# Optimization experiments

Hardware: AMD Instinct MI355X
Metric: run time of the kernel (lower is better)

## Reference

```python
import jax, jax.numpy as jnp
import numpy as np

HID = 2048      # hidden_size
NH = 32         # num_heads
G = 8           # num_kv_groups
R = NH // G     # repeat factor (heads per kv group)
HD = HID // NH  # head_dim = 64
SCALE = HD ** 0.5


def setup_inputs() -> dict:
    key = jax.random.key(0)
    ks = jax.random.split(key, 10)
    B, S = 2, 1024
    x = jax.random.normal(ks[0], (B, S, HID), dtype=jnp.float32)
    attention_mask = jnp.ones((B, S, S), dtype=jnp.float32)
    # Linear params stored as [in, out] (y = x @ W + b), same math as torch Linear.
    Wq = jax.random.normal(ks[1], (HID, HID), dtype=jnp.float32) * 0.02
    bq = jnp.zeros((HID,), dtype=jnp.float32)
    Wk = jax.random.normal(ks[2], (HID, G * HD), dtype=jnp.float32) * 0.02
    bk = jnp.zeros((G * HD,), dtype=jnp.float32)
    Wv = jax.random.normal(ks[3], (HID, G * HD), dtype=jnp.float32) * 0.02
    bv = jnp.zeros((G * HD,), dtype=jnp.float32)
    Wo = jax.random.normal(ks[4], (HID, HID), dtype=jnp.float32) * 0.02
    bo = jnp.zeros((HID,), dtype=jnp.float32)
    return {"x": x, "attention_mask": attention_mask,
            "Wq": Wq, "bq": bq, "Wk": Wk, "bk": bk,
            "Wv": Wv, "bv": bv, "Wo": Wo, "bo": bo}


def reference(x, attention_mask, Wq, bq, Wk, bk, Wv, bv, Wo, bo):
    B, S, _ = x.shape
    # Projections. Group heads as (G, R) instead of repeat_interleave:
    # repeat_interleave(key, R, dim=2) duplicates each kv group R times, which is
    # exactly sharing key[:, :, g] across the R heads of group g.
    q = (x @ Wq + bq).reshape(B, S, G, R, HD)   # [B,S,G,R,HD] (heads = G*R in order)
    k = (x @ Wk + bk).reshape(B, S, G, HD)      # [B,S,G,HD]
    v = (x @ Wv + bv).reshape(B, S, G, HD)
    # scores [B,G,R,Sq,Sk] == torch's [B, NH, Sq, Sk] with NH = G*R
    scores = jnp.einsum('bqgrd,bkgd->bgrqk', q, k) / SCALE
    scores = scores * attention_mask[:, None, None]  # multiplicative mask per head
    w = jax.nn.softmax(scores, axis=-1)
    out = jnp.einsum('bgrqk,bkgd->bqgrd', w, v).reshape(B, S, HID)
    return out @ Wo + bo + x
```

## Files before the change

### kernel.cpp

```cpp
#include <hip/hip_runtime.h>

typedef unsigned short u16;
typedef unsigned int u32;
typedef __attribute__((ext_vector_type(8))) short bf16x8;
typedef __attribute__((ext_vector_type(4))) float f32x4;

#define HID 2048
#define S_LEN 1024
#define BATCH 2
#define G_KV 8
#define R_REP 4
#define HD 64
#define NQKV 3072

__device__ __forceinline__ u16 f2bf(float f) {
    union { u32 u; float ff; } x; x.ff = f;
    u32 u = x.u;
    u += 0x7FFFu + ((u >> 16) & 1u);
    return (u16)(u >> 16);
}

__device__ __forceinline__ void gload_lds16(const void* g, void* l) {
    __builtin_amdgcn_global_load_lds((const __attribute__((address_space(1))) void*)g,
                                     (__attribute__((address_space(3))) void*)l,
                                     16, 0, 0);
}

__global__ __launch_bounds__(256) void cvt_x(const float* __restrict__ in,
                                             u16* __restrict__ out) {
    int i = (blockIdx.x * 256 + threadIdx.x) * 8;
    float4 a = *(const float4*)(in + i);
    float4 b = *(const float4*)(in + i + 4);
    u16 t[8] = {f2bf(a.x), f2bf(a.y), f2bf(a.z), f2bf(a.w),
                f2bf(b.x), f2bf(b.y), f2bf(b.z), f2bf(b.w)};
    *(uint4*)(out + i) = *(const uint4*)t;
}

__global__ __launch_bounds__(256) void mask_perm(const float* __restrict__ mask,
                                                 float* __restrict__ out) {
    __shared__ float tile[64 * 68];
    int bid = blockIdx.x;
    int kt = bid & 15, qblk = (bid >> 4) & 15, b = bid >> 8;
    int t = threadIdx.x;
    int row = t >> 2, c0 = (t & 3) * 16;
    const float* src = mask + ((size_t)b * S_LEN + qblk * 64 + row) * S_LEN + kt * 64 + c0;
#pragma unroll
    for (int i = 0; i < 4; ++i)
        *(float4*)&tile[row * 68 + c0 + i * 4] = *(const float4*)(src + i * 4);
    __syncthreads();
    int w = t >> 6, quad = (t >> 4) & 3, l16 = t & 15;
    int q = w * 16 + l16;
    float* dst = out + (size_t)bid * 4096 + t * 16;
#pragma unroll
    for (int mt = 0; mt < 4; ++mt) {
        float4 v = *(const float4*)&tile[q * 68 + mt * 16 + quad * 4];
        *(float4*)(dst + mt * 4) = v;
    }
}

__global__ __launch_bounds__(256) void transpose_qkv(const float* __restrict__ Wq,
                                                     const float* __restrict__ Wk,
                                                     const float* __restrict__ Wv,
                                                     u16* __restrict__ out) {
    __shared__ float tile[32][33];
    int n0 = blockIdx.x * 32, k0 = blockIdx.y * 32;
    const float* in; int N, nc0;
    if (n0 < 2048)      { in = Wq; N = 2048; nc0 = n0; }
    else if (n0 < 2560) { in = Wk; N = 512;  nc0 = n0 - 2048; }
    else                { in = Wv; N = 512;  nc0 = n0 - 2560; }
    int tx = threadIdx.x, ty = threadIdx.y;
#pragma unroll
    for (int j = 0; j < 4; ++j)
        tile[ty + j * 8][tx] = in[(size_t)(k0 + ty + j * 8) * N + nc0 + tx];
    __syncthreads();
#pragma unroll
    for (int j = 0; j < 4; ++j)
        out[(size_t)(n0 + ty + j * 8) * 2048 + k0 + tx] = f2bf(tile[tx][ty + j * 8]);
}

__global__ __launch_bounds__(256) void transpose_cvt(const float* __restrict__ in,
                                                     u16* __restrict__ out,
                                                     int K, int N) {
    __shared__ float tile[32][33];
    int n0 = blockIdx.x * 32, k0 = blockIdx.y * 32;
    int tx = threadIdx.x, ty = threadIdx.y;
#pragma unroll
    for (int j = 0; j < 4; ++j)
        tile[ty + j * 8][tx] = in[(size_t)(k0 + ty + j * 8) * N + n0 + tx];
    __syncthreads();
#pragma unroll
    for (int j = 0; j < 4; ++j)
        out[(size_t)(n0 + ty + j * 8) * K + k0 + tx] = f2bf(tile[tx][ty + j * 8]);
}

__global__ __launch_bounds__(256) void gemm_qkv(const u16* __restrict__ Xb,
                                                const u16* __restrict__ WT,
                                                const float* __restrict__ bq,
                                                const float* __restrict__ bk,
                                                const float* __restrict__ bv,
                                                u16* __restrict__ qb,
                                                u16* __restrict__ kb,
                                                u16* __restrict__ vb) {
    __shared__ __align__(16) u16 As[64 * 32];
    __shared__ __align__(16) u16 Bs[128 * 32];
    int tid = threadIdx.x;
    int w = tid >> 6, lane = tid & 63, quad = lane >> 4, l16 = lane & 15;
    int m0 = blockIdx.y * 64, n0 = blockIdx.x * 128;
    int wr = (w >> 1) * 32, wc = (w & 1) * 64;
    int srow = lane >> 2, scol = (lane & 3) * 8;

    f32x4 acc[2][4];
#pragma unroll
    for (int i = 0; i < 2; ++i)
#pragma unroll
        for (int j = 0; j < 4; ++j) acc[i][j] = (f32x4){0.f, 0.f, 0.f, 0.f};

    for (int k0 = 0; k0 < 2048; k0 += 32) {
        gload_lds16(&Xb[(size_t)(m0 + w * 16 + srow) * 2048 + k0 + scol], &As[(w * 16) * 32]);
#pragma unroll
        for (int c = 0; c < 2; ++c) {
            int row = w * 32 + c * 16;
            gload_lds16(&WT[(size_t)(n0 + row + srow) * 2048 + k0 + scol], &Bs[row * 32]);
        }
        __syncthreads();
        bf16x8 af[2], bfr[4];
#pragma unroll
        for (int mt = 0; mt < 2; ++mt)
            af[mt] = *(const bf16x8*)&As[(wr + mt * 16 + l16) * 32 + quad * 8];
#pragma unroll
        for (int nt = 0; nt < 4; ++nt)
            bfr[nt] = *(const bf16x8*)&Bs[(wc + nt * 16 + l16) * 32 + quad * 8];
#pragma unroll
        for (int mt = 0; mt < 2; ++mt)
#pragma unroll
            for (int nt = 0; nt < 4; ++nt)
                acc[mt][nt] = __builtin_amdgcn_mfma_f32_16x16x32_bf16(af[mt], bfr[nt], acc[mt][nt], 0, 0, 0);
        __syncthreads();
    }

#pragma unroll
    for (int nt = 0; nt < 4; ++nt) {
        int n = n0 + wc + nt * 16 + l16;
        float bias;
        if (n < 2048) bias = bq[n];
        else if (n < 2560) bias = bk[n - 2048];
        else bias = bv[n - 2560];
#pragma unroll
        for (int mt = 0; mt < 2; ++mt) {
#pragma unroll
            for (int reg = 0; reg < 4; ++reg) {
                int m = m0 + wr + mt * 16 + quad * 4 + reg;
                float val = acc[mt][nt][reg] + bias;
                int b = m >> 10, s = m & 1023;
                if (n < 2048) {
                    int g = n >> 8, r = (n >> 6) & 3, d = n & 63;
                    qb[((((size_t)(b * G_KV + g) * R_REP + r) * S_LEN) + s) * HD + d] = f2bf(val * 0.125f);
                } else if (n < 2560) {
                    int n2 = n - 2048, g = n2 >> 6, d = n2 & 63;
                    kb[(((size_t)(b * G_KV + g) * S_LEN) + s) * HD + d] = f2bf(val);
                } else {
                    int n2 = n - 2560, g = n2 >> 6, d = n2 & 63;
                    vb[(((size_t)(b * G_KV + g) * HD + d) * S_LEN) + s] = f2bf(val);
                }
            }
        }
    }
}

__global__ __launch_bounds__(256) void attn_mfma(const u16* __restrict__ qbuf,
                                                 const u16* __restrict__ kbuf,
                                                 const u16* __restrict__ vtbuf,
                                                 const float* __restrict__ mask_pm,
                                                 u16* __restrict__ aout) {
    __shared__ __align__(16) u16 Ks[64 * 72];
    __shared__ __align__(16) u16 Vs[64 * 72];
    __shared__ __align__(16) u16 Ps[64 * 72];
    __shared__ float l_lds[64];

    int d = blockIdx.x;
    int xcd = d & 7, j = d >> 3;
    int pr = xcd * 2 + (j >> 6);
    int r = (j >> 4) & 3, qblk = j & 15;
    int b = pr >> 3, g = pr & 7;

    int tid = threadIdx.x;
    int w = tid >> 6, lane = tid & 63, quad = lane >> 4, l16 = lane & 15;
    int s0 = qblk * 64;
    int q = w * 16 + l16;

    const u16* qrow = qbuf +
        ((((size_t)(b * G_KV + g) * R_REP + r) * S_LEN) + s0 + q) * HD;
    bf16x8 qf0 = *(const bf16x8*)(qrow + quad * 8);
    bf16x8 qf1 = *(const bf16x8*)(qrow + 32 + quad * 8);

    f32x4 o_acc[4];
#pragma unroll
    for (int i = 0; i < 4; ++i) o_acc[i] = (f32x4){0.f, 0.f, 0.f, 0.f};
    float l_part = 0.f;

    const u16* kbase  = kbuf  + (size_t)(b * G_KV + g) * S_LEN * HD;
    const u16* vtbase = vtbuf + (size_t)(b * G_KV + g) * HD * S_LEN;
    const float* mbase = mask_pm + ((size_t)(b * 16 + qblk) * 16) * 4096 + tid * 16;

    int srow = tid >> 2, sc = (tid & 3) * 16;

    uint4 kp0, kp1, vp0, vp1;
    f32x4 mc[4], mn[4];
    {
        const u16* kr = kbase + (size_t)srow * HD + sc;
        kp0 = *(const uint4*)kr; kp1 = *(const uint4*)(kr + 8);
        const u16* vr = vtbase + (size_t)srow * S_LEN + sc;
        vp0 = *(const uint4*)vr; vp1 = *(const uint4*)(vr + 8);
#pragma unroll
        for (int i = 0; i < 4; ++i) mc[i] = *(const f32x4*)(mbase + i * 4);
    }

    for (int kt = 0; kt < 16; ++kt) {
        __syncthreads();
        *(uint4*)&Ks[srow * 72 + sc]     = kp0;
        *(uint4*)&Ks[srow * 72 + sc + 8] = kp1;
        *(uint4*)&Vs[srow * 72 + sc]     = vp0;
        *(uint4*)&Vs[srow * 72 + sc + 8] = vp1;
        __syncthreads();

        if (kt < 15) {
            int nk = (kt + 1) * 64;
            const u16* kr = kbase + (size_t)(nk + srow) * HD + sc;
            kp0 = *(const uint4*)kr; kp1 = *(const uint4*)(kr + 8);
            const u16* vr = vtbase + (size_t)srow * S_LEN + nk + sc;
            vp0 = *(const uint4*)vr; vp1 = *(const uint4*)(vr + 8);
            const float* mr = mbase + (size_t)(kt + 1) * 4096;
#pragma unroll
            for (int i = 0; i < 4; ++i) mn[i] = *(const f32x4*)(mr + i * 4);
        }

#pragma unroll
        for (int mt = 0; mt < 4; ++mt) {
            bf16x8 af0 = *(const bf16x8*)&Ks[(mt * 16 + l16) * 72 + quad * 8];
            bf16x8 af1 = *(const bf16x8*)&Ks[(mt * 16 + l16) * 72 + 32 + quad * 8];
            f32x4 z = (f32x4){0.f, 0.f, 0.f, 0.f};
            z = __builtin_amdgcn_mfma_f32_16x16x32_bf16(af0, qf0, z, 0, 0, 0);
            f32x4 s = __builtin_amdgcn_mfma_f32_16x16x32_bf16(af1, qf1, s = z, 0, 0, 0);

            u32 er[4];
#pragma unroll
            for (int rg = 0; rg < 4; ++rg) {
                float e = __expf(s[rg] * mc[mt][rg]);
                u32 u = __float_as_uint(e) + 0x8000u;
                er[rg] = u;
                l_part += __uint_as_float(u & 0xFFFF0000u);
            }
            uint2 pk;
            pk.x = __builtin_amdgcn_perm(er[1], er[0], 0x07060302u);
            pk.y = __builtin_amdgcn_perm(er[3], er[2], 0x07060302u);
            *(uint2*)&Ps[q * 72 + mt * 16 + quad * 4] = pk;
        }

        bf16x8 pf0 = *(const bf16x8*)&Ps[q * 72 + quad * 8];
        bf16x8 pf1 = *(const bf16x8*)&Ps[q * 72 + 32 + quad * 8];
#pragma unroll
        for (int nt = 0; nt < 4; ++nt) {
            bf16x8 vf0 = *(const bf16x8*)&Vs[(nt * 16 + l16) * 72 + quad * 8];
            bf16x8 vf1 = *(const bf16x8*)&Vs[(nt * 16 + l16) * 72 + 32 + quad * 8];
            o_acc[nt] = __builtin_amdgcn_mfma_f32_16x16x32_bf16(pf0, vf0, o_acc[nt], 0, 0, 0);
            o_acc[nt] = __builtin_amdgcn_mfma_f32_16x16x32_bf16(pf1, vf1, o_acc[nt], 0, 0, 0);
        }
#pragma unroll
        for (int i = 0; i < 4; ++i) mc[i] = mn[i];
    }

    l_part += __shfl_xor(l_part, 16);
    l_part += __shfl_xor(l_part, 32);
    l_lds[w * 16 + l16] = l_part;

#pragma unroll
    for (int reg = 0; reg < 4; ++reg) {
        int row = w * 16 + quad * 4 + reg;
        float inv = 1.0f / l_lds[row];
        int sidx = s0 + row;
        u16* dst = aout + ((size_t)(b * S_LEN + sidx)) * HID + (g * R_REP + r) * HD;
#pragma unroll
        for (int nt = 0; nt < 4; ++nt)
            dst[nt * 16 + l16] = f2bf(o_acc[nt][reg] * inv);
    }
}

__global__ __launch_bounds__(256) void gemm_o(const u16* __restrict__ A,
                                              const u16* __restrict__ WT,
                                              const float* __restrict__ bo,
                                              const float* __restrict__ Xres,
                                              float* __restrict__ out) {
    __shared__ __align__(16) u16 As[64 * 32];
    __shared__ __align__(16) u16 Bs[128 * 32];
    int tid = threadIdx.x;
    int w = tid >> 6, lane = tid & 63, quad = lane >> 4, l16 = lane & 15;
    int m0 = blockIdx.y * 64, n0 = blockIdx.x * 128;
    int wr = (w >> 1) * 32, wc = (w & 1) * 64;
    int srow = lane >> 2, scol = (lane & 3) * 8;

    f32x4 acc[2][4];
#pragma unroll
    for (int i = 0; i < 2; ++i)
#pragma unroll
        for (int j = 0; j < 4; ++j) acc[i][j] = (f32x4){0.f, 0.f, 0.f, 0.f};

    for (int k0 = 0; k0 < 2048; k0 += 32) {
        gload_lds16(&A[(size_t)(m0 + w * 16 + srow) * 2048 + k0 + scol], &As[(w * 16) * 32]);
#pragma unroll
        for (int c = 0; c < 2; ++c) {
            int row = w * 32 + c * 16;
            gload_lds16(&WT[(size_t)(n0 + row + srow) * 2048 + k0 + scol], &Bs[row * 32]);
        }
        __syncthreads();
        bf16x8 af[2], bfr[4];
#pragma unroll
        for (int mt = 0; mt < 2; ++mt)
            af[mt] = *(const bf16x8*)&As[(wr + mt * 16 + l16) * 32 + quad * 8];
#pragma unroll
        for (int nt = 0; nt < 4; ++nt)
            bfr[nt] = *(const bf16x8*)&Bs[(wc + nt * 16 + l16) * 32 + quad * 8];
#pragma unroll
        for (int mt = 0; mt < 2; ++mt)
#pragma unroll
            for (int nt = 0; nt < 4; ++nt)
                acc[mt][nt] = __builtin_amdgcn_mfma_f32_16x16x32_bf16(af[mt], bfr[nt], acc[mt][nt], 0, 0, 0);
        __syncthreads();
    }

#pragma unroll
    for (int nt = 0; nt < 4; ++nt) {
        int n = n0 + wc + nt * 16 + l16;
        float bias = bo[n];
#pragma unroll
        for (int mt = 0; mt < 2; ++mt) {
#pragma unroll
            for (int reg = 0; reg < 4; ++reg) {
                int m = m0 + wr + mt * 16 + quad * 4 + reg;
                out[(size_t)m * 2048 + n] = acc[mt][nt][reg] + bias + Xres[(size_t)m * 2048 + n];
            }
        }
    }
}

extern "C" void kernel_launch(void* const* d_in, const int* in_sizes, int n_in,
                              void* d_out, int out_size, void* d_ws, size_t ws_size,
                              hipStream_t stream) {
    const float* x    = (const float*)d_in[0];
    const float* mask = (const float*)d_in[1];
    const float* Wq   = (const float*)d_in[2];
    const float* bq   = (const float*)d_in[3];
    const float* Wk   = (const float*)d_in[4];
    const float* bk   = (const float*)d_in[5];
    const float* Wv   = (const float*)d_in[6];
    const float* bv   = (const float*)d_in[7];
    const float* Wo   = (const float*)d_in[8];
    const float* bo   = (const float*)d_in[9];
    float* out = (float*)d_out;

    u16* ws = (u16*)d_ws;
    size_t off = 0;
    u16* WqkvT = ws + off; off += (size_t)NQKV * 2048;
    u16* WoT   = ws + off; off += (size_t)2048 * 2048;
    u16* q_buf = ws + off; off += (size_t)BATCH * G_KV * R_REP * S_LEN * HD;
    u16* k_buf = ws + off; off += (size_t)BATCH * G_KV * S_LEN * HD;
    u16* v_buf = ws + off; off += (size_t)BATCH * G_KV * S_LEN * HD;
    u16* a_out = ws + off; off += (size_t)2048 * 2048;
    u16* Xb       = a_out;
    float* mask_pm = (float*)WqkvT;

    cvt_x<<<dim3(2048 * 2048 / (256 * 8)), 256, 0, stream>>>(x, Xb);

    dim3 tb(32, 8);
    transpose_qkv<<<dim3(96, 64), tb, 0, stream>>>(Wq, Wk, Wv, WqkvT);
    transpose_cvt<<<dim3(64, 64), tb, 0, stream>>>(Wo, WoT, 2048, 2048);

    gemm_qkv<<<dim3(NQKV / 128, 2048 / 64), 256, 0, stream>>>(Xb, WqkvT, bq, bk, bv,
                                                              q_buf, k_buf, v_buf);

    mask_perm<<<dim3(BATCH * 16 * 16), 256, 0, stream>>>(mask, mask_pm);

    attn_mfma<<<dim3(BATCH * G_KV * R_REP * (S_LEN / 64)), 256, 0, stream>>>(
        q_buf, k_buf, v_buf, mask_pm, a_out);

    gemm_o<<<dim3(2048 / 128, 2048 / 64), 256, 0, stream>>>(a_out, WoT, bo, x, out);
}
```

Before: 242.6 us.

## Fuse prep kernels, double-buffer GEMM K-tiles, read mask directly in attention

Merges the x conversion and both weight transpose/convert kernels into one launch, so fewer kernels are launched. Both GEMMs now use double-buffered LDS tiles with K=64, prefetching the next tile while MFMAs consume the current one, which halves the barrier count per K. The mask permutation kernel is removed and attention reads the original mask rows directly, saving a full mask rewrite pass at the cost of less contiguous per-thread mask loads. The larger LDS footprint may reduce GEMM occupancy.

```diff
diff --git a/kernel.cpp b/kernel.cpp
--- a/kernel.cpp
+++ b/kernel.cpp
@@ -26,71 +26,56 @@
                                      16, 0, 0);
 }
 
-__global__ __launch_bounds__(256) void cvt_x(const float* __restrict__ in,
-                                             u16* __restrict__ out) {
-    int i = (blockIdx.x * 256 + threadIdx.x) * 8;
-    float4 a = *(const float4*)(in + i);
-    float4 b = *(const float4*)(in + i + 4);
-    u16 t[8] = {f2bf(a.x), f2bf(a.y), f2bf(a.z), f2bf(a.w),
-                f2bf(b.x), f2bf(b.y), f2bf(b.z), f2bf(b.w)};
-    *(uint4*)(out + i) = *(const uint4*)t;
-}
-
-__global__ __launch_bounds__(256) void mask_perm(const float* __restrict__ mask,
-                                                 float* __restrict__ out) {
-    __shared__ float tile[64 * 68];
-    int bid = blockIdx.x;
-    int kt = bid & 15, qblk = (bid >> 4) & 15, b = bid >> 8;
-    int t = threadIdx.x;
-    int row = t >> 2, c0 = (t & 3) * 16;
-    const float* src = mask + ((size_t)b * S_LEN + qblk * 64 + row) * S_LEN + kt * 64 + c0;
-#pragma unroll
-    for (int i = 0; i < 4; ++i)
-        *(float4*)&tile[row * 68 + c0 + i * 4] = *(const float4*)(src + i * 4);
-    __syncthreads();
-    int w = t >> 6, quad = (t >> 4) & 3, l16 = t & 15;
-    int q = w * 16 + l16;
-    float* dst = out + (size_t)bid * 4096 + t * 16;
-#pragma unroll
-    for (int mt = 0; mt < 4; ++mt) {
-        float4 v = *(const float4*)&tile[q * 68 + mt * 16 + quad * 4];
-        *(float4*)(dst + mt * 4) = v;
-    }
-}
-
-__global__ __launch_bounds__(256) void transpose_qkv(const float* __restrict__ Wq,
-                                                     const float* __restrict__ Wk,
-                                                     const float* __restrict__ Wv,
-                                                     u16* __restrict__ out) {
+__global__ __launch_bounds__(256) void prep(const float* __restrict__ x,
+                                            const float* __restrict__ Wq,
+                                            const float* __restrict__ Wk,
+                                            const float* __restrict__ Wv,
+                                            const float* __restrict__ Wo,
+                                            u16* __restrict__ Xb,
+                                            u16* __restrict__ WqkvT,
+                                            u16* __restrict__ WoT) {
     __shared__ float tile[32][33];
-    int n0 = blockIdx.x * 32, k0 = blockIdx.y * 32;
-    const float* in; int N, nc0;
-    if (n0 < 2048)      { in = Wq; N = 2048; nc0 = n0; }
-    else if (n0 < 2560) { in = Wk; N = 512;  nc0 = n0 - 2048; }
-    else                { in = Wv; N = 512;  nc0 = n0 - 2560; }
-    int tx = threadIdx.x, ty = threadIdx.y;
-#pragma unroll
-    for (int j = 0; j < 4; ++j)
-        tile[ty + j * 8][tx] = in[(size_t)(k0 + ty + j * 8) * N + nc0 + tx];
-    __syncthreads();
-#pragma unroll
-    for (int j = 0; j < 4; ++j)
-        out[(size_t)(n0 + ty + j * 8) * 2048 + k0 + tx] = f2bf(tile[tx][ty + j * 8]);
-}
-
-__global__ __launch_bounds__(256) void transpose_cvt(const float* __restrict__ in,
-                                                     u16* __restrict__ out,
-                                                     int K, int N) {
-    __shared__ float tile[32][33];
-    int n0 = blockIdx.x * 32, k0 = blockIdx.y * 32;
-    int tx = threadIdx.x, ty = threadIdx.y;
-#pragma unroll
-    for (int j = 0; j < 4; ++j)
-        tile[ty + j * 8][tx] = in[(size_t)(k0 + ty + j * 8) * N + n0 + tx];
-    __syncthreads();
-#pragma unroll
-    for (int j = 0; j < 4; ++j)
-        out[(size_t)(n0 + ty + j * 8) * K + k0 + tx] = f2bf(tile[tx][ty + j * 8]);
+    int bid = blockIdx.x, tid = threadIdx.x;
+
+    if (bid < 2048) {
+        int i = (bid * 256 + tid) * 8;
+        float4 a = *(const float4*)(x + i);
+        float4 b = *(const float4*)(x + i + 4);
+        u16 t[8] = {f2bf(a.x), f2bf(a.y), f2bf(a.z), f2bf(a.w),
+                    f2bf(b.x), f2bf(b.y), f2bf(b.z), f2bf(b.w)};
+        *(uint4*)(Xb + i) = *(const uint4*)t;
+        return;
+    }
+
+    int tx = tid & 31, ty = tid >> 5;
+    if (bid < 8192) {
+        int local = bid - 2048;
+        int n0 = (local % 96) * 32, k0 = (local / 96) * 32;
+        const float* in; int N, nc0;
+        if (n0 < 2048)      { in = Wq; N = 2048; nc0 = n0; }
+        else if (n0 < 2560) { in = Wk; N = 512;  nc0 = n0 - 2048; }
+        else                { in = Wv; N = 512;  nc0 = n0 - 2560; }
+#pragma unroll
+        for (int j = 0; j < 4; ++j)
+            tile[ty + j * 8][tx] = in[(size_t)(k0 + ty + j * 8) * N + nc0 + tx];
+        __syncthreads();
+#pragma unroll
+        for (int j = 0; j < 4; ++j)
+            WqkvT[(size_t)(n0 + ty + j * 8) * 2048 + k0 + tx] = f2bf(tile[tx][ty + j * 8]);
+        return;
+    }
+
+    {
+        int local = bid - 8192;
+        int n0 = (local & 63) * 32, k0 = (local >> 6) * 32;
+#pragma unroll
+        for (int j = 0; j < 4; ++j)
+            tile[ty + j * 8][tx] = Wo[(size_t)(k0 + ty + j * 8) * 2048 + n0 + tx];
+        __syncthreads();
+#pragma unroll
+        for (int j = 0; j < 4; ++j)
+            WoT[(size_t)(n0 + ty + j * 8) * 2048 + k0 + tx] = f2bf(tile[tx][ty + j * 8]);
+    }
 }
 
 __global__ __launch_bounds__(256) void gemm_qkv(const u16* __restrict__ Xb,
@@ -101,13 +86,17 @@
                                                 u16* __restrict__ qb,
                                                 u16* __restrict__ kb,
                                                 u16* __restrict__ vb) {
-    __shared__ __align__(16) u16 As[64 * 32];
-    __shared__ __align__(16) u16 Bs[128 * 32];
+    __shared__ __align__(16) u16 As[2][64 * 64];
+    __shared__ __align__(16) u16 Bs[2][128 * 64];
     int tid = threadIdx.x;
     int w = tid >> 6, lane = tid & 63, quad = lane >> 4, l16 = lane & 15;
     int m0 = blockIdx.y * 64, n0 = blockIdx.x * 128;
     int wr = (w >> 1) * 32, wc = (w & 1) * 64;
-    int srow = lane >> 2, scol = (lane & 3) * 8;
+    int srow = lane >> 3, scol = (lane & 7) * 8;
+
+    const u16* aP0 = &Xb[(size_t)(m0 + w * 16 + srow) * 2048 + scol];
+    const u16* aP1 = aP0 + (size_t)8 * 2048;
+    const u16* bP  = &WT[(size_t)(n0 + w * 32 + srow) * 2048 + scol];
 
     f32x4 acc[2][4];
 #pragma unroll
@@ -115,27 +104,40 @@
 #pragma unroll
         for (int j = 0; j < 4; ++j) acc[i][j] = (f32x4){0.f, 0.f, 0.f, 0.f};
 
-    for (int k0 = 0; k0 < 2048; k0 += 32) {
-        gload_lds16(&Xb[(size_t)(m0 + w * 16 + srow) * 2048 + k0 + scol], &As[(w * 16) * 32]);
-#pragma unroll
-        for (int c = 0; c < 2; ++c) {
-            int row = w * 32 + c * 16;
-            gload_lds16(&WT[(size_t)(n0 + row + srow) * 2048 + k0 + scol], &Bs[row * 32]);
-        }
-        __syncthreads();
-        bf16x8 af[2], bfr[4];
-#pragma unroll
-        for (int mt = 0; mt < 2; ++mt)
-            af[mt] = *(const bf16x8*)&As[(wr + mt * 16 + l16) * 32 + quad * 8];
-#pragma unroll
-        for (int nt = 0; nt < 4; ++nt)
-            bfr[nt] = *(const bf16x8*)&Bs[(wc + nt * 16 + l16) * 32 + quad * 8];
-#pragma unroll
-        for (int mt = 0; mt < 2; ++mt)
+    gload_lds16(aP0, &As[0][(w * 16) * 64]);
+    gload_lds16(aP1, &As[0][(w * 16 + 8) * 64]);
+#pragma unroll
+    for (int j = 0; j < 4; ++j)
+        gload_lds16(bP + (size_t)(j * 8) * 2048, &Bs[0][(w * 32 + j * 8) * 64]);
+    __syncthreads();
+
+    int cur = 0;
+    for (int k0 = 0; k0 < 2048; k0 += 64) {
+        int kn = k0 + 64;
+        if (kn < 2048) {
+            gload_lds16(aP0 + kn, &As[cur ^ 1][(w * 16) * 64]);
+            gload_lds16(aP1 + kn, &As[cur ^ 1][(w * 16 + 8) * 64]);
+#pragma unroll
+            for (int j = 0; j < 4; ++j)
+                gload_lds16(bP + (size_t)(j * 8) * 2048 + kn, &Bs[cur ^ 1][(w * 32 + j * 8) * 64]);
+        }
+#pragma unroll
+        for (int kk = 0; kk < 2; ++kk) {
+            bf16x8 af[2], bfr[4];
+#pragma unroll
+            for (int mt = 0; mt < 2; ++mt)
+                af[mt] = *(const bf16x8*)&As[cur][(wr + mt * 16 + l16) * 64 + kk * 32 + quad * 8];
 #pragma unroll
             for (int nt = 0; nt < 4; ++nt)
-                acc[mt][nt] = __builtin_amdgcn_mfma_f32_16x16x32_bf16(af[mt], bfr[nt], acc[mt][nt], 0, 0, 0);
-        __syncthreads();
+                bfr[nt] = *(const bf16x8*)&Bs[cur][(wc + nt * 16 + l16) * 64 + kk * 32 + quad * 8];
+#pragma unroll
+            for (int mt = 0; mt < 2; ++mt)
+#pragma unroll
+                for (int nt = 0; nt < 4; ++nt)
+                    acc[mt][nt] = __builtin_amdgcn_mfma_f32_16x16x32_bf16(af[mt], bfr[nt], acc[mt][nt], 0, 0, 0);
+        }
+        __syncthreads();
+        cur ^= 1;
     }
 
 #pragma unroll
@@ -170,7 +172,7 @@
 __global__ __launch_bounds__(256) void attn_mfma(const u16* __restrict__ qbuf,
                                                  const u16* __restrict__ kbuf,
                                                  const u16* __restrict__ vtbuf,
-                                                 const float* __restrict__ mask_pm,
+                                                 const float* __restrict__ mask,
                                                  u16* __restrict__ aout) {
     __shared__ __align__(16) u16 Ks[64 * 72];
     __shared__ __align__(16) u16 Vs[64 * 72];
@@ -200,7 +202,7 @@
 
     const u16* kbase  = kbuf  + (size_t)(b * G_KV + g) * S_LEN * HD;
     const u16* vtbase = vtbuf + (size_t)(b * G_KV + g) * HD * S_LEN;
-    const float* mbase = mask_pm + ((size_t)(b * 16 + qblk) * 16) * 4096 + tid * 16;
+    const float* mrow = mask + ((size_t)b * S_LEN + s0 + q) * S_LEN + quad * 4;
 
     int srow = tid >> 2, sc = (tid & 3) * 16;
 
@@ -212,7 +214,7 @@
         const u16* vr = vtbase + (size_t)srow * S_LEN + sc;
         vp0 = *(const uint4*)vr; vp1 = *(const uint4*)(vr + 8);
 #pragma unroll
-        for (int i = 0; i < 4; ++i) mc[i] = *(const f32x4*)(mbase + i * 4);
+        for (int i = 0; i < 4; ++i) mc[i] = *(const f32x4*)(mrow + i * 16);
     }
 
     for (int kt = 0; kt < 16; ++kt) {
@@ -229,9 +231,9 @@
             kp0 = *(const uint4*)kr; kp1 = *(const uint4*)(kr + 8);
             const u16* vr = vtbase + (size_t)srow * S_LEN + nk + sc;
             vp0 = *(const uint4*)vr; vp1 = *(const uint4*)(vr + 8);
-            const float* mr = mbase + (size_t)(kt + 1) * 4096;
-#pragma unroll
-            for (int i = 0; i < 4; ++i) mn[i] = *(const f32x4*)(mr + i * 4);
+            const float* mr = mrow + nk;
+#pragma unroll
+            for (int i = 0; i < 4; ++i) mn[i] = *(const f32x4*)(mr + i * 16);
         }
 
 #pragma unroll
@@ -290,13 +292,17 @@
                                               const float* __restrict__ bo,
                                               const float* __restrict__ Xres,
                                               float* __restrict__ out) {
-    __shared__ __align__(16) u16 As[64 * 32];
-    __shared__ __align__(16) u16 Bs[128 * 32];
+    __shared__ __align__(16) u16 As[2][64 * 64];
+    __shared__ __align__(16) u16 Bs[2][128 * 64];
     int tid = threadIdx.x;
     int w = tid >> 6, lane = tid & 63, quad = lane >> 4, l16 = lane & 15;
     int m0 = blockIdx.y * 64, n0 = blockIdx.x * 128;
     int wr = (w >> 1) * 32, wc = (w & 1) * 64;
-    int srow = lane >> 2, scol = (lane & 3) * 8;
+    int srow = lane >> 3, scol = (lane & 7) * 8;
+
+    const u16* aP0 = &A[(size_t)(m0 + w * 16 + srow) * 2048 + scol];
+    const u16* aP1 = aP0 + (size_t)8 * 2048;
+    const u16* bP  = &WT[(size_t)(n0 + w * 32 + srow) * 2048 + scol];
 
     f32x4 acc[2][4];
 #pragma unroll
@@ -304,27 +310,40 @@
 #pragma unroll
         for (int j = 0; j < 4; ++j) acc[i][j] = (f32x4){0.f, 0.f, 0.f, 0.f};
 
-    for (int k0 = 0; k0 < 2048; k0 += 32) {
-        gload_lds16(&A[(size_t)(m0 + w * 16 + srow) * 2048 + k0 + scol], &As[(w * 16) * 32]);
-#pragma unroll
-        for (int c = 0; c < 2; ++c) {
-            int row = w * 32 + c * 16;
-            gload_lds16(&WT[(size_t)(n0 + row + srow) * 2048 + k0 + scol], &Bs[row * 32]);
-        }
-        __syncthreads();
-        bf16x8 af[2], bfr[4];
-#pragma unroll
-        for (int mt = 0; mt < 2; ++mt)
-            af[mt] = *(const bf16x8*)&As[(wr + mt * 16 + l16) * 32 + quad * 8];
-#pragma unroll
-        for (int nt = 0; nt < 4; ++nt)
-            bfr[nt] = *(const bf16x8*)&Bs[(wc + nt * 16 + l16) * 32 + quad * 8];
-#pragma unroll
-        for (int mt = 0; mt < 2; ++mt)
+    gload_lds16(aP0, &As[0][(w * 16) * 64]);
+    gload_lds16(aP1, &As[0][(w * 16 + 8) * 64]);
+#pragma unroll
+    for (int j = 0; j < 4; ++j)
+        gload_lds16(bP + (size_t)(j * 8) * 2048, &Bs[0][(w * 32 + j * 8) * 64]);
+    __syncthreads();
+
+    int cur = 0;
+    for (int k0 = 0; k0 < 2048; k0 += 64) {
+        int kn = k0 + 64;
+        if (kn < 2048) {
+            gload_lds16(aP0 + kn, &As[cur ^ 1][(w * 16) * 64]);
+            gload_lds16(aP1 + kn, &As[cur ^ 1][(w * 16 + 8) * 64]);
+#pragma unroll
+            for (int j = 0; j < 4; ++j)
+                gload_lds16(bP + (size_t)(j * 8) * 2048 + kn, &Bs[cur ^ 1][(w * 32 + j * 8) * 64]);
+        }
+#pragma unroll
+        for (int kk = 0; kk < 2; ++kk) {
+            bf16x8 af[2], bfr[4];
+#pragma unroll
+            for (int mt = 0; mt < 2; ++mt)
+                af[mt] = *(const bf16x8*)&As[cur][(wr + mt * 16 + l16) * 64 + kk * 32 + quad * 8];
 #pragma unroll
             for (int nt = 0; nt < 4; ++nt)
-                acc[mt][nt] = __builtin_amdgcn_mfma_f32_16x16x32_bf16(af[mt], bfr[nt], acc[mt][nt], 0, 0, 0);
-        __syncthreads();
+                bfr[nt] = *(const bf16x8*)&Bs[cur][(wc + nt * 16 + l16) * 64 + kk * 32 + quad * 8];
+#pragma unroll
+            for (int mt = 0; mt < 2; ++mt)
+#pragma unroll
+                for (int nt = 0; nt < 4; ++nt)
+                    acc[mt][nt] = __builtin_amdgcn_mfma_f32_16x16x32_bf16(af[mt], bfr[nt], acc[mt][nt], 0, 0, 0);
+        }
+        __syncthreads();
+        cur ^= 1;
     }
 
 #pragma unroll
@@ -365,22 +384,15 @@
     u16* k_buf = ws + off; off += (size_t)BATCH * G_KV * S_LEN * HD;
     u16* v_buf = ws + off; off += (size_t)BATCH * G_KV * S_LEN * HD;
     u16* a_out = ws + off; off += (size_t)2048 * 2048;
-    u16* Xb       = a_out;
-    float* mask_pm = (float*)WqkvT;
-
-    cvt_x<<<dim3(2048 * 2048 / (256 * 8)), 256, 0, stream>>>(x, Xb);
-
-    dim3 tb(32, 8);
-    transpose_qkv<<<dim3(96, 64), tb, 0, stream>>>(Wq, Wk, Wv, WqkvT);
-    transpose_cvt<<<dim3(64, 64), tb, 0, stream>>>(Wo, WoT, 2048, 2048);
+    u16* Xb    = a_out;
+
+    prep<<<dim3(12288), 256, 0, stream>>>(x, Wq, Wk, Wv, Wo, Xb, WqkvT, WoT);
 
     gemm_qkv<<<dim3(NQKV / 128, 2048 / 64), 256, 0, stream>>>(Xb, WqkvT, bq, bk, bv,
                                                               q_buf, k_buf, v_buf);
 
-    mask_perm<<<dim3(BATCH * 16 * 16), 256, 0, stream>>>(mask, mask_pm);
-
     attn_mfma<<<dim3(BATCH * G_KV * R_REP * (S_LEN / 64)), 256, 0, stream>>>(
-        q_buf, k_buf, v_buf, mask_pm, a_out);
+        q_buf, k_buf, v_buf, mask, a_out);
 
     gemm_o<<<dim3(2048 / 128, 2048 / 64), 256, 0, stream>>>(a_out, WoT, bo, x, out);
 }
```

After: 252.7 us. 4.2% more time.
